# Performance work log

Hardware: AMD Instinct MI355X
Metric: run time of the kernel (lower is better)

## Reference

```python
import jax, jax.numpy as jnp
import numpy as np
from jax import lax

D_MODEL, D_STATE, D_CONV, EXPAND, HEADDIM = 1024, 128, 4, 2, 64
D_INNER = EXPAND * D_MODEL            # 2048
NHEADS = D_INNER // HEADDIM           # 32
CONV_DIM = D_INNER + 2 * D_STATE      # 2304 (ngroups=1)
D_IN_PROJ = 2 * D_INNER + 2 * D_STATE + NHEADS  # 4384


def setup_inputs() -> dict:
    key = jax.random.key(0)
    ks = jax.random.split(key, 9)
    b, l = 2, 2048
    x = jax.random.normal(ks[0], (b, l, D_MODEL), jnp.float32)
    in_proj_w = jax.random.normal(ks[1], (D_IN_PROJ, D_MODEL), jnp.float32) * 0.02
    conv_w = jax.random.normal(ks[2], (CONV_DIM, D_CONV), jnp.float32) * 0.2
    conv_b = jax.random.normal(ks[3], (CONV_DIM,), jnp.float32) * 0.02
    dt_bias = jnp.log(jnp.expm1(jax.random.uniform(ks[4], (NHEADS,), jnp.float32, 0.001, 0.1)))
    A_log = jnp.log(jax.random.uniform(ks[5], (NHEADS,), jnp.float32, 1.0, 16.0))
    D = jax.random.normal(ks[6], (NHEADS,), jnp.float32)
    norm_w = jnp.ones((D_INNER,), jnp.float32)
    out_proj_w = jax.random.normal(ks[7], (D_MODEL, D_INNER), jnp.float32) * 0.02
    return {"x": x, "in_proj_w": in_proj_w, "conv_w": conv_w, "conv_b": conv_b,
            "dt_bias": dt_bias, "A_log": A_log, "D": D, "norm_w": norm_w,
            "out_proj_w": out_proj_w}


def _mamba2(x, in_proj_w, conv_w, conv_b, dt_bias, A_log, D, norm_w, out_proj_w):
    b, l, _ = x.shape
    zxbcdt = x @ in_proj_w.T  # (b,l,D_IN_PROJ)
    z = zxbcdt[..., :D_INNER]
    xBC = zxbcdt[..., D_INNER:D_INNER + CONV_DIM]
    dt = zxbcdt[..., D_INNER + CONV_DIM:]  # (b,l,h)
    # causal depthwise conv1d + SiLU
    xBC_pad = jnp.pad(xBC, ((0, 0), (D_CONV - 1, 0), (0, 0)))
    windows = jnp.stack([xBC_pad[:, k:k + l, :] for k in range(D_CONV)], axis=-1)  # (b,l,c,K)
    xBC = jax.nn.silu(jnp.einsum('blck,ck->blc', windows, conv_w) + conv_b)
    xs = xBC[..., :D_INNER]
    B = xBC[..., D_INNER:D_INNER + D_STATE]   # (b,l,n)
    C = xBC[..., D_INNER + D_STATE:]          # (b,l,n)
    xh = xs.reshape(b, l, NHEADS, HEADDIM)
    dt = jax.nn.softplus(dt + dt_bias)        # (b,l,h)
    A = -jnp.exp(A_log)                       # (h,)
    dA = jnp.exp(dt * A)                      # (b,l,h)
    xdt = xh * dt[..., None]                  # (b,l,h,p)

    def step(S, inp):
        dA_t, xdt_t, B_t, C_t = inp  # (b,h),(b,h,p),(b,n),(b,n)
        S = dA_t[:, :, None, None] * S + xdt_t[..., None] * B_t[:, None, None, :]
        y_t = jnp.einsum('bhpn,bn->bhp', S, C_t)
        return S, y_t

    S0 = jnp.zeros((b, NHEADS, HEADDIM, D_STATE), x.dtype)
    _, y = lax.scan(step, S0,
                    (dA.transpose(1, 0, 2), xdt.transpose(1, 0, 2, 3),
                     B.transpose(1, 0, 2), C.transpose(1, 0, 2)))
    y = y.transpose(1, 0, 2, 3) + D[None, None, :, None] * xh  # (b,l,h,p)
    y = y.reshape(b, l, D_INNER)
    # gated RMSNorm: norm(y * silu(z)) * weight
    y = y * jax.nn.silu(z)
    y = y * lax.rsqrt(jnp.mean(y * y, axis=-1, keepdims=True) + 1e-5) * norm_w
    return y @ out_proj_w.T


def reference(x, in_proj_w, conv_w, conv_b, dt_bias, A_log, D, norm_w, out_proj_w):
    return x + _mamba2(x, in_proj_w, conv_w, conv_b, dt_bias, A_log, D, norm_w, out_proj_w)
```

## Files before the change

kernel.cpp:

```cpp
#include <hip/hip_runtime.h>
#include <hip/hip_bf16.h>
#include <cstdint>

typedef __hip_bfloat16 bf16;
typedef __attribute__((ext_vector_type(8))) short short8;
typedef __attribute__((ext_vector_type(4))) float f32x4;
typedef unsigned int u32;

#define BB 2
#define LL 2048
#define DM 1024
#define DI 2048
#define DS 128
#define NH 32
#define HD 64
#define CONVD 2304
#define DPROJ 4384
#define DPAD 4480
#define NBL (BB*LL)
#define NCHK 16
#define CLEN 128

__device__ __forceinline__ float bf2f(bf16 v) { return __bfloat162float(v); }
__device__ __forceinline__ bf16 f2bf(float f) { return __float2bfloat16(f); }
__device__ __forceinline__ unsigned short f2bfu(float f) {
  bf16 t = __float2bfloat16(f); return *(unsigned short*)&t;
}
__device__ __forceinline__ float bfu2f(unsigned short u) {
  u32 b = ((u32)u) << 16; return *(float*)&b;
}

__device__ __forceinline__ void gload16(const void* g, void* l) {
  __builtin_amdgcn_global_load_lds(
      (const __attribute__((address_space(1))) u32*)g,
      (__attribute__((address_space(3))) u32*)l, 16, 0, 0);
}

template<int N> __device__ __forceinline__ void waitvm() {
  __builtin_amdgcn_sched_barrier(0);
  if constexpr (N == 0) asm volatile("s_waitcnt vmcnt(0)" ::: "memory");
  else if constexpr (N == 3) asm volatile("s_waitcnt vmcnt(3)" ::: "memory");
  else if constexpr (N == 4) asm volatile("s_waitcnt vmcnt(4)" ::: "memory");
  __builtin_amdgcn_sched_barrier(0);
}
__device__ __forceinline__ void rawbar() {
  __builtin_amdgcn_sched_barrier(0);
  __builtin_amdgcn_s_barrier();
  __builtin_amdgcn_sched_barrier(0);
}

__global__ __launch_bounds__(256)
void k_cast3(const float* __restrict__ s0, bf16* __restrict__ d0, int n0,
             const float* __restrict__ s1, bf16* __restrict__ d1, int n1,
             const float* __restrict__ s2, bf16* __restrict__ d2, int n2)
{
  int i = blockIdx.x * blockDim.x + threadIdx.x;
  const int stride = gridDim.x * blockDim.x;
  const int total = n0 + n1 + n2;
  for (; i < total; i += stride) {
    const float* s; bf16* d; int j = i;
    if (j < n0)            { s = s0; d = d0; }
    else if (j < n0 + n1)  { s = s1; d = d1; j -= n0; }
    else                   { s = s2; d = d2; j -= n0 + n1; }
    const float4 v = ((const float4*)s)[j];
    u32 w0 = (u32)f2bfu(v.x) | ((u32)f2bfu(v.y) << 16);
    u32 w1 = (u32)f2bfu(v.z) | ((u32)f2bfu(v.w) << 16);
    *(uint2*)(d + (size_t)j*4) = make_uint2(w0, w1);
  }
}

template<int TM, int MODE>
__global__ __launch_bounds__(512)
void k_gemm_nt(const bf16* __restrict__ A, const bf16* __restrict__ W,
               int K, int Nw, int ldo,
               float* __restrict__ outf, const bf16* __restrict__ residb,
               bf16* __restrict__ outb, float* __restrict__ dtraw)
{
  constexpr int BUFE = (TM + 128) * 64;
  constexpr int LPT  = TM/64 + 2;
  __shared__ __align__(16) unsigned short S[3*BUFE];
  const int tid = threadIdx.x;
  const int w = tid >> 6, lane = tid & 63;
  const int m0 = blockIdx.x * TM, n0 = blockIdx.y * 128;
  const int wr = w >> 2, wc = w & 3;
  constexpr int MI = TM / 32;
  f32x4 acc[MI][2] = {};
  const int r0 = lane & 15;
  const int kq = (lane >> 4) * 8;
  const int srow = lane >> 3;
  const int scol = ((lane & 7) ^ (lane >> 3)) << 3;
  const int swz  = (r0 & 7) << 3;
  const int NT = K >> 6;

#define STAGE(T, BUF) {                                                          \
    const int k0s = (T) << 6;                                                    \
    unsigned short* dst = S + (BUF) * BUFE;                                      \
    _Pragma("unroll")                                                            \
    for (int it = 0; it < TM/64; ++it) {                                         \
      const int seg = it*8 + w;                                                  \
      const int row = seg*8 + srow;                                              \
      gload16(A + (size_t)(m0 + row)*K + (k0s + scol), (char*)dst + seg*1024);   \
    }                                                                            \
    unsigned short* dstW = dst + TM*64;                                          \
    _Pragma("unroll")                                                            \
    for (int it = 0; it < 2; ++it) {                                             \
      const int seg = it*8 + w;                                                  \
      const int row = seg*8 + srow;                                              \
      int rw = n0 + row; rw = (rw < Nw) ? rw : (Nw - 1);                         \
      gload16(W + (size_t)rw*K + (k0s + scol), (char*)dstW + seg*1024);          \
    }                                                                            \
  }

  STAGE(0, 0);
  STAGE(1, 1);
  waitvm<LPT>();
  rawbar();

  for (int t = 0; t < NT; ++t) {
    const int cur = t % 3;
    if (t + 2 < NT) STAGE(t + 2, (t + 2) % 3);
    const unsigned short* As = S + cur*BUFE;
    const unsigned short* Ws = As + TM*64;
    __builtin_amdgcn_s_setprio(1);
    #pragma unroll
    for (int kk = 0; kk < 64; kk += 32) {
      const int ce = (kk + kq) ^ swz;
      short8 af[MI], bw[2];
      #pragma unroll
      for (int mi = 0; mi < MI; ++mi)
        af[mi] = *(const short8*)(As + (wr*(TM/2) + mi*16 + r0)*64 + ce);
      #pragma unroll
      for (int ni = 0; ni < 2; ++ni)
        bw[ni] = *(const short8*)(Ws + (wc*32 + ni*16 + r0)*64 + ce);
      #pragma unroll
      for (int mi = 0; mi < MI; ++mi)
        #pragma unroll
        for (int ni = 0; ni < 2; ++ni)
          acc[mi][ni] = __builtin_amdgcn_mfma_f32_16x16x32_bf16(af[mi], bw[ni], acc[mi][ni], 0, 0, 0);
    }
    __builtin_amdgcn_s_setprio(0);
    if (t + 1 < NT) {
      if (t + 2 < NT) waitvm<LPT>();
      else            waitvm<0>();
      rawbar();
    }
  }
#undef STAGE

  const int rr = (lane >> 4) * 4;
  if (MODE == 0) {
    #pragma unroll
    for (int mi = 0; mi < MI; ++mi) {
      #pragma unroll
      for (int ni = 0; ni < 2; ++ni) {
        const int col = n0 + wc*32 + ni*16 + r0;
        #pragma unroll
        for (int r = 0; r < 4; ++r) {
          const int row = m0 + wr*(TM/2) + mi*16 + rr + r;
          outf[(size_t)row*ldo + col] =
              acc[mi][ni][r] + bf2f(residb[(size_t)row*ldo + col]);
        }
      }
    }
  } else {
    if (n0 == 4352 && wc == 0) {
      #pragma unroll
      for (int ni = 0; ni < 2; ++ni)
        #pragma unroll
        for (int mi = 0; mi < MI; ++mi)
          #pragma unroll
          for (int r = 0; r < 4; ++r) {
            const int row = m0 + wr*(TM/2) + mi*16 + rr + r;
            dtraw[(size_t)row*NH + ni*16 + r0] = acc[mi][ni][r];
          }
    }
    __syncthreads();
    #pragma unroll
    for (int mi = 0; mi < MI; ++mi) {
      #pragma unroll
      for (int ni = 0; ni < 2; ++ni) {
        const int colt = wc*32 + ni*16 + r0;
        #pragma unroll
        for (int r = 0; r < 4; ++r) {
          const int rowt = wr*(TM/2) + mi*16 + rr + r;
          const int g = (colt >> 3) ^ (rowt & 7);
          S[rowt*128 + g*8 + (colt & 7)] = f2bfu(acc[mi][ni][r]);
        }
      }
    }
    __syncthreads();
    const int row = tid >> 2, j4 = tid & 3;
    unsigned short* orow = (unsigned short*)outb + (size_t)(m0 + row)*ldo + n0 + j4*32;
    #pragma unroll
    for (int jj = 0; jj < 4; ++jj) {
      const int g = (j4*4 + jj) ^ (row & 7);
      *(short8*)(orow + jj*8) = *(const short8*)&S[row*128 + g*8];
    }
  }
}

__global__ __launch_bounds__(256)
void k_conv(const bf16* __restrict__ zxb, const float* __restrict__ dtraw,
            const float* __restrict__ convw, const float* __restrict__ convb,
            const float* __restrict__ dtb, const float* __restrict__ alog,
            bf16* __restrict__ xs, float* __restrict__ dt,
            float* __restrict__ ldA, bf16* __restrict__ Bc, bf16* __restrict__ Cc)
{
  const int bl = ((blockIdx.x & 7) << 9) | (blockIdx.x >> 3);
  const int l = bl & (LL - 1);
  const int tid = threadIdx.x;
  if (tid < NH) {
    float raw = dtraw[(size_t)bl*NH + tid] + dtb[tid];
    float sp = (raw > 20.f) ? raw : log1pf(__expf(raw));
    float Ah = -__expf(alog[tid]);
    dt[(size_t)bl*NH + tid] = sp;
    ldA[(size_t)bl*NH + tid] = sp * Ah;
  }
  for (int g = tid; g < CONVD/8; g += 256) {
    const int c0 = g*8;
    float acc[8];
    float4 wv[8];
    #pragma unroll
    for (int e = 0; e < 8; ++e) wv[e] = ((const float4*)convw)[c0 + e];
    {
      const float4 b0 = *(const float4*)(convb + c0);
      const float4 b1 = *(const float4*)(convb + c0 + 4);
      acc[0]=b0.x; acc[1]=b0.y; acc[2]=b0.z; acc[3]=b0.w;
      acc[4]=b1.x; acc[5]=b1.y; acc[6]=b1.z; acc[7]=b1.w;
    }
    #pragma unroll
    for (int k = 0; k < 4; ++k) {
      if (l - 3 + k >= 0) {
        short8 v = *(const short8*)((const unsigned short*)zxb + (size_t)(bl - 3 + k)*DPAD + DI + c0);
        #pragma unroll
        for (int e = 0; e < 8; ++e) {
          const float wk = (k == 0) ? wv[e].x : (k == 1) ? wv[e].y : (k == 2) ? wv[e].z : wv[e].w;
          acc[e] = fmaf(bfu2f((unsigned short)v[e]), wk, acc[e]);
        }
      }
    }
    short8 ov;
    #pragma unroll
    for (int e = 0; e < 8; ++e) {
      const float s = acc[e] / (1.f + __expf(-acc[e]));
      ov[e] = (short)f2bfu(s);
    }
    if (c0 < DI)            *(short8*)((unsigned short*)xs + (size_t)bl*DI + c0) = ov;
    else if (c0 < DI + DS)  *(short8*)((unsigned short*)Bc + (size_t)bl*DS + (c0 - DI)) = ov;
    else                    *(short8*)((unsigned short*)Cc + (size_t)bl*DS + (c0 - DI - DS)) = ov;
  }
}

__global__ __launch_bounds__(256)
void k_bt(const bf16* __restrict__ Bc, bf16* __restrict__ BT)
{
  const int bidx2 = blockIdx.x;
  const int b = bidx2 >> 4, c = bidx2 & 15;
  const int bl0 = b*LL + c*CLEN;
  __shared__ unsigned short LT[128*132];
  const int tid = threadIdx.x;
  {
    const int ts = tid >> 3, seg = tid & 7;
    #pragma unroll
    for (int r = 0; r < 4; ++r) {
      const int t = r*32 + ts;
      const unsigned short* src = (const unsigned short*)(Bc + (size_t)(bl0 + t)*DS);
      short8 v0 = *(const short8*)(src + seg*16);
      short8 v1 = *(const short8*)(src + seg*16 + 8);
      u32 w0 = (u32)(unsigned short)v0[0] | ((u32)(unsigned short)v0[1] << 16);
      u32 w1 = (u32)(unsigned short)v0[2] | ((u32)(unsigned short)v0[3] << 16);
      u32 w2 = (u32)(unsigned short)v0[4] | ((u32)(unsigned short)v0[5] << 16);
      u32 w3 = (u32)(unsigned short)v0[6] | ((u32)(unsigned short)v0[7] << 16);
      u32 w4 = (u32)(unsigned short)v1[0] | ((u32)(unsigned short)v1[1] << 16);
      u32 w5 = (u32)(unsigned short)v1[2] | ((u32)(unsigned short)v1[3] << 16);
      u32 w6 = (u32)(unsigned short)v1[4] | ((u32)(unsigned short)v1[5] << 16);
      u32 w7 = (u32)(unsigned short)v1[6] | ((u32)(unsigned short)v1[7] << 16);
      uint2* d = (uint2*)&LT[t*132 + seg*16];
      d[0] = make_uint2(w0, w1); d[1] = make_uint2(w2, w3);
      d[2] = make_uint2(w4, w5); d[3] = make_uint2(w6, w7);
    }
  }
  __syncthreads();
  {
    const int n = tid >> 1, th = tid & 1;
    unsigned short* dst = (unsigned short*)(BT + (size_t)bidx2*16384 + n*128 + th*64);
    #pragma unroll
    for (int j = 0; j < 8; ++j) {
      short8 o;
      #pragma unroll
      for (int e = 0; e < 8; ++e)
        o[e] = (short)LT[(th*64 + j*8 + e)*132 + n];
      *(short8*)(dst + j*8) = o;
    }
  }
}

__global__ __launch_bounds__(512)
void k_xt_state(const bf16* __restrict__ xs, const float* __restrict__ dt,
                const bf16* __restrict__ BT, const float* __restrict__ ldA,
                bf16* __restrict__ xT, unsigned short* __restrict__ Sloc,
                float* __restrict__ clog)
{
  const int bidx = blockIdx.x;
  const int c = bidx & 15, h = (bidx >> 4) & 31, b = bidx >> 9;
  const int bl0 = b*LL + c*CLEN;
  const int bidx2 = b*NCHK + c;
  __shared__ unsigned short LT[128*68];
  __shared__ __align__(16) unsigned short XWs[64*136];
  __shared__ float w1[128];
  const int tid = threadIdx.x;
  const int w = tid >> 6, lane = tid & 63;
  const int r0 = lane & 15, kq = (lane >> 4) * 8;
  short8 bfr[4];
  #pragma unroll
  for (int kk = 0; kk < 4; ++kk)
    bfr[kk] = *(const short8*)((const unsigned short*)BT + (size_t)bidx2*16384
                               + (size_t)(w*16 + r0)*128 + kk*32 + kq);
  {
    const int ts = tid >> 3, seg = tid & 7;
    #pragma unroll
    for (int r = 0; r < 2; ++r) {
      const int t = r*64 + ts;
      const float dtv = dt[(size_t)(bl0 + t)*NH + h];
      short8 v = *(const short8*)((const unsigned short*)(xs + (size_t)(bl0 + t)*DI + h*HD) + seg*8);
      unsigned short o[8];
      #pragma unroll
      for (int e = 0; e < 8; ++e)
        o[e] = f2bfu(bfu2f((unsigned short)v[e]) * dtv);
      uint2* d = (uint2*)&LT[t*68 + seg*8];
      d[0] = make_uint2((u32)o[0] | ((u32)o[1] << 16), (u32)o[2] | ((u32)o[3] << 16));
      d[1] = make_uint2((u32)o[4] | ((u32)o[5] << 16), (u32)o[6] | ((u32)o[7] << 16));
    }
  }
  if (tid < 64) {
    const int ln = tid;
    const float a0 = ldA[(size_t)(bl0 + 2*ln)*NH + h];
    const float a1 = ldA[(size_t)(bl0 + 2*ln + 1)*NH + h];
    float s = a0 + a1;
    #pragma unroll
    for (int off = 1; off < 64; off <<= 1) {
      const float v = __shfl_up(s, off);
      if (ln >= off) s += v;
    }
    const float Ltot = __shfl(s, 63);
    w1[2*ln + 1] = __expf(Ltot - s);
    w1[2*ln]     = __expf(Ltot - (s - a1));
    if (ln == 63) clog[bidx] = Ltot;
  }
  __syncthreads();
  {
    const int p = tid >> 3, tg = tid & 7;
    unsigned short* xdst = (unsigned short*)xT + (size_t)bidx*8192 + p*128 + tg*16;
    #pragma unroll
    for (int half = 0; half < 2; ++half) {
      short8 oXT, oXW;
      #pragma unroll
      for (int e = 0; e < 8; ++e) {
        const int t = tg*16 + half*8 + e;
        const unsigned short u = LT[t*68 + p];
        oXT[e] = (short)u;
        oXW[e] = (short)f2bfu(bfu2f(u) * w1[t]);
      }
      *(short8*)(xdst + half*8) = oXT;
      *(short8*)&XWs[p*136 + tg*16 + half*8] = oXW;
    }
  }
  __syncthreads();
  f32x4 acc[4] = {};
  #pragma unroll
  for (int kk = 0; kk < 4; ++kk) {
    #pragma unroll
    for (int mi = 0; mi < 4; ++mi) {
      short8 a = *(const short8*)&XWs[(mi*16 + r0)*136 + kk*32 + kq];
      acc[mi] = __builtin_amdgcn_mfma_f32_16x16x32_bf16(a, bfr[kk], acc[mi], 0, 0, 0);
    }
  }
  const int rr = (lane >> 4) * 4;
  unsigned short* So = Sloc + (size_t)bidx*8192;
  #pragma unroll
  for (int mi = 0; mi < 4; ++mi)
    #pragma unroll
    for (int r = 0; r < 4; ++r)
      So[(mi*16 + rr + r)*128 + w*16 + r0] = f2bfu(acc[mi][r]);
}

__global__ __launch_bounds__(256)
void k_chunk_combine(unsigned short* __restrict__ Sloc, const float* __restrict__ clog)
{
  const int bh = blockIdx.x >> 3;
  const int e0 = ((blockIdx.x & 7) * 256 + threadIdx.x) * 4;
  float t0 = 0.f, t1 = 0.f, t2 = 0.f, t3 = 0.f;
  for (int c = 0; c < NCHK; ++c) {
    unsigned short* Sp = Sloc + ((size_t)(bh*NCHK + c))*8192 + e0;
    const uint2 raw = *(const uint2*)Sp;
    const float l0 = bfu2f((unsigned short)(raw.x & 0xffff));
    const float l1 = bfu2f((unsigned short)(raw.x >> 16));
    const float l2 = bfu2f((unsigned short)(raw.y & 0xffff));
    const float l3 = bfu2f((unsigned short)(raw.y >> 16));
    uint2 o;
    o.x = (u32)f2bfu(t0) | ((u32)f2bfu(t1) << 16);
    o.y = (u32)f2bfu(t2) | ((u32)f2bfu(t3) << 16);
    *(uint2*)Sp = o;
    const float P = __expf(clog[bh*NCHK + c]);
    t0 = P*t0 + l0; t1 = P*t1 + l1; t2 = P*t2 + l2; t3 = P*t3 + l3;
  }
}

__global__ __launch_bounds__(512)
void k_scan(const bf16* __restrict__ xT, const bf16* __restrict__ Bc,
            const bf16* __restrict__ Cc, const unsigned short* __restrict__ Sinit,
            const float* __restrict__ ldA, const bf16* __restrict__ xs,
            const float* __restrict__ Dv, unsigned short* __restrict__ y)
{
  const int bidx = blockIdx.x;
  const int c = bidx & 15, h = (bidx >> 4) & 31, b = bidx >> 9;
  const int bl0 = b*LL + c*CLEN;
  __shared__ __align__(16) unsigned short Bs[128*136];
  __shared__ __align__(16) unsigned short XDs[64*136];
  __shared__ __align__(16) unsigned short SIs[64*136];
  __shared__ float la[128];
  const int tid = threadIdx.x;
  const int w = tid >> 6, lane = tid & 63;
  const int r0 = lane & 15, kq = (lane >> 4) * 8;
  short8 cfr[4];
  #pragma unroll
  for (int kk = 0; kk < 4; ++kk)
    cfr[kk] = *(const short8*)((const unsigned short*)Cc
                               + (size_t)(bl0 + w*16 + r0)*DS + kk*32 + kq);
  {
    const int t = tid >> 2, sg = tid & 3;
    const unsigned short* sb = (const unsigned short*)(Bc + (size_t)(bl0 + t)*DS) + sg*32;
    #pragma unroll
    for (int j = 0; j < 4; ++j)
      *(short8*)&Bs[t*136 + sg*32 + j*8] = *(const short8*)(sb + j*8);
  }
  {
    const int p = tid >> 3, seg = tid & 7;
    const unsigned short* sx = (const unsigned short*)(xT + (size_t)bidx*8192 + p*128) + seg*16;
    *(short8*)&XDs[p*136 + seg*16]     = *(const short8*)sx;
    *(short8*)&XDs[p*136 + seg*16 + 8] = *(const short8*)(sx + 8);
    const unsigned short* sp = Sinit + (size_t)bidx*8192 + p*128 + seg*16;
    *(short8*)&SIs[p*136 + seg*16]     = *(const short8*)sp;
    *(short8*)&SIs[p*136 + seg*16 + 8] = *(const short8*)(sp + 8);
  }
  if (tid < 64) {
    const int ln = tid;
    const float a0 = ldA[(size_t)(bl0 + 2*ln)*NH + h];
    const float a1 = ldA[(size_t)(bl0 + 2*ln + 1)*NH + h];
    float s = a0 + a1;
    #pragma unroll
    for (int off = 1; off < 64; off <<= 1) {
      const float v = __shfl_up(s, off);
      if (ln >= off) s += v;
    }
    la[2*ln + 1] = s;
    la[2*ln]     = s - a1;
  }
  __syncthreads();

  const int trow = w*16 + (lane >> 4) * 4;

  f32x4 aG[8] = {};
  f32x4 aU[4] = {};
  #pragma unroll
  for (int kk = 0; kk < 4; ++kk) {
    #pragma unroll
    for (int sf = 0; sf < 8; ++sf) {
      short8 bb = *(const short8*)&Bs[(sf*16 + r0)*136 + kk*32 + kq];
      aG[sf] = __builtin_amdgcn_mfma_f32_16x16x32_bf16(cfr[kk], bb, aG[sf], 0, 0, 0);
    }
    #pragma unroll
    for (int pf = 0; pf < 4; ++pf) {
      short8 bs = *(const short8*)&SIs[(pf*16 + r0)*136 + kk*32 + kq];
      aU[pf] = __builtin_amdgcn_mfma_f32_16x16x32_bf16(cfr[kk], bs, aU[pf], 0, 0, 0);
    }
  }
  __syncthreads();
  float lat[4];
  #pragma unroll
  for (int r = 0; r < 4; ++r) lat[r] = la[trow + r];
  #pragma unroll
  for (int sf = 0; sf < 8; ++sf) {
    const int s = sf*16 + r0;
    const float las = la[s];
    #pragma unroll
    for (int r = 0; r < 4; ++r) {
      const int t = trow + r;
      const float m = (s <= t) ? aG[sf][r] * __expf(lat[r] - las) : 0.f;
      Bs[t*136 + s] = f2bfu(m);
    }
  }
  __syncthreads();
  f32x4 aY[4] = {};
  #pragma unroll
  for (int kk = 0; kk < 4; ++kk) {
    short8 a = *(const short8*)&Bs[(w*16 + r0)*136 + kk*32 + kq];
    #pragma unroll
    for (int pf = 0; pf < 4; ++pf) {
      short8 bx = *(const short8*)&XDs[(pf*16 + r0)*136 + kk*32 + kq];
      aY[pf] = __builtin_amdgcn_mfma_f32_16x16x32_bf16(a, bx, aY[pf], 0, 0, 0);
    }
  }
  const float Dh = Dv[h];
  float el[4];
  #pragma unroll
  for (int r = 0; r < 4; ++r) el[r] = __expf(lat[r]);
  #pragma unroll
  for (int pf = 0; pf < 4; ++pf) {
    #pragma unroll
    for (int r = 0; r < 4; ++r) {
      const int t = trow + r, p = pf*16 + r0;
      const size_t gi = (size_t)(bl0 + t)*DI + h*HD + p;
      const float yv = aY[pf][r] + el[r]*aU[pf][r] + Dh*bfu2f(((const unsigned short*)xs)[gi]);
      y[gi] = f2bfu(yv);
    }
  }
}

__global__ __launch_bounds__(256)
void k_gate_norm(const unsigned short* __restrict__ y, const bf16* __restrict__ zxb,
                 const float* __restrict__ nw, bf16* __restrict__ yn)
{
  const size_t bl = blockIdx.x;
  const int tid = threadIdx.x;
  const int c0 = tid * 8;
  short8 yv8 = *(const short8*)(y + bl*DI + c0);
  short8 zv = *(const short8*)((const unsigned short*)zxb + bl*DPAD + c0);
  float v[8];
  float acc = 0.f;
  #pragma unroll
  for (int e = 0; e < 8; ++e) {
    const float zf = bfu2f((unsigned short)zv[e]);
    v[e] = bfu2f((unsigned short)yv8[e]) * (zf / (1.f + __expf(-zf)));
    acc += v[e]*v[e];
  }
  #pragma unroll
  for (int off = 32; off > 0; off >>= 1) acc += __shfl_down(acc, off);
  __shared__ float red[4];
  if ((tid & 63) == 0) red[tid >> 6] = acc;
  __syncthreads();
  const float total = red[0] + red[1] + red[2] + red[3];
  const float r = rsqrtf(total * (1.f/DI) + 1e-5f);
  const float4 w0 = *(const float4*)(nw + c0);
  const float4 w1 = *(const float4*)(nw + c0 + 4);
  const float wv[8] = {w0.x, w0.y, w0.z, w0.w, w1.x, w1.y, w1.z, w1.w};
  short8 ov;
  #pragma unroll
  for (int e = 0; e < 8; ++e) ov[e] = (short)f2bfu(v[e] * r * wv[e]);
  *(short8*)((unsigned short*)yn + bl*DI + c0) = ov;
}

extern "C" void kernel_launch(void* const* d_in, const int* in_sizes, int n_in,
                              void* d_out, int out_size, void* d_ws, size_t ws_size,
                              hipStream_t stream)
{
  const float* x     = (const float*)d_in[0];
  const float* inw   = (const float*)d_in[1];
  const float* convw = (const float*)d_in[2];
  const float* convb = (const float*)d_in[3];
  const float* dtb   = (const float*)d_in[4];
  const float* alog  = (const float*)d_in[5];
  const float* Dv    = (const float*)d_in[6];
  const float* nw    = (const float*)d_in[7];
  const float* outw  = (const float*)d_in[8];
  float* out = (float*)d_out;
  char* ws = (char*)d_ws;

  constexpr size_t OFF_ZX   = 0;
  constexpr size_t OFF_DTRAW= OFF_ZX   + (size_t)NBL*DPAD*2;
  constexpr size_t OFF_XS   = OFF_DTRAW+ (size_t)NBL*NH*4;
  constexpr size_t OFF_DT   = OFF_XS   + (size_t)NBL*DI*2;
  constexpr size_t OFF_LDA  = OFF_DT   + (size_t)NBL*NH*4;
  constexpr size_t OFF_B    = OFF_LDA  + (size_t)NBL*NH*4;
  constexpr size_t OFF_C    = OFF_B    + (size_t)NBL*DS*2;
  constexpr size_t OFF_XT   = OFF_C    + (size_t)NBL*DS*2;
  constexpr size_t OFF_BT   = OFF_XT   + (size_t)1024*8192*2;
  constexpr size_t OFF_SLOC = OFF_BT   + (size_t)32*16384*2;
  constexpr size_t OFF_CLOG = OFF_SLOC + (size_t)1024*8192*2;
  constexpr size_t OFF_Y    = OFF_CLOG + 4096;
  constexpr size_t OFF_YN   = OFF_Y    + (size_t)NBL*DI*2;
  constexpr size_t OFF_XB   = OFF_YN   + (size_t)NBL*DI*2;
  constexpr size_t OFF_INWB = OFF_XB   + (size_t)NBL*DM*2;
  constexpr size_t OFF_OUTWB= OFF_INWB + (size_t)DPROJ*DM*2;

  bf16*  zxb  = (bf16*) (ws + OFF_ZX);
  float* dtraw= (float*)(ws + OFF_DTRAW);
  bf16*  xs   = (bf16*) (ws + OFF_XS);
  float* dt   = (float*)(ws + OFF_DT);
  float* ldA  = (float*)(ws + OFF_LDA);
  bf16*  Bcp  = (bf16*) (ws + OFF_B);
  bf16*  Ccp  = (bf16*) (ws + OFF_C);
  bf16*  xT   = (bf16*) (ws + OFF_XT);
  bf16*  BT   = (bf16*) (ws + OFF_BT);
  unsigned short* Sloc = (unsigned short*)(ws + OFF_SLOC);
  float* clog = (float*)(ws + OFF_CLOG);
  unsigned short* yb = (unsigned short*)(ws + OFF_Y);
  bf16*  yn   = (bf16*) (ws + OFF_YN);
  bf16*  xb   = (bf16*) (ws + OFF_XB);
  bf16*  inwb = (bf16*) (ws + OFF_INWB);
  bf16*  outwb= (bf16*) (ws + OFF_OUTWB);

  k_cast3<<<2048, 256, 0, stream>>>(x, xb, NBL*DM/4,
                                    inw, inwb, DPROJ*DM/4,
                                    outw, outwb, DM*DI/4);
  k_gemm_nt<128,1><<<dim3(32, 35), 512, 0, stream>>>(xb, inwb, DM, DPROJ, DPAD, nullptr, nullptr, zxb, dtraw);
  k_conv<<<NBL, 256, 0, stream>>>(zxb, dtraw, convw, convb, dtb, alog, xs, dt, ldA, Bcp, Ccp);
  k_bt<<<BB*NCHK, 256, 0, stream>>>(Bcp, BT);
  k_xt_state<<<BB*NH*NCHK, 512, 0, stream>>>(xs, dt, BT, ldA, xT, Sloc, clog);
  k_chunk_combine<<<64*8, 256, 0, stream>>>(Sloc, clog);
  k_scan<<<BB*NH*NCHK, 512, 0, stream>>>(xT, Bcp, Ccp, Sloc, ldA, xs, Dv, yb);
  k_gate_norm<<<NBL, 256, 0, stream>>>(yb, zxb, nw, yn);
  k_gemm_nt<64,0><<<dim3(64, 8), 512, 0, stream>>>(yn, outwb, DI, DM, DM, out, xb, nullptr, nullptr);
}
```

Measured before the change: 203.9 us.

## Load in-projection A operand directly to registers and raise MFMA priority in scan kernels

Adds a dedicated in-projection GEMM kernel that loads the activation tile straight from global memory into registers, double-buffered across even and odd K steps. Only the weight tile is staged through LDS, which shrinks LDS use and may allow more resident blocks (launch bounds now request 4). The scan and state kernels also wrap their MFMA loops in s_setprio to favour matrix issue. The cost is higher register pressure from direct global loads, which are not coalesced the way the LDS staging was.

```diff
diff --git a/kernel.cpp b/kernel.cpp
--- a/kernel.cpp
+++ b/kernel.cpp
@@ -39,6 +39,7 @@
 template<int N> __device__ __forceinline__ void waitvm() {
   __builtin_amdgcn_sched_barrier(0);
   if constexpr (N == 0) asm volatile("s_waitcnt vmcnt(0)" ::: "memory");
+  else if constexpr (N == 2) asm volatile("s_waitcnt vmcnt(2)" ::: "memory");
   else if constexpr (N == 3) asm volatile("s_waitcnt vmcnt(3)" ::: "memory");
   else if constexpr (N == 4) asm volatile("s_waitcnt vmcnt(4)" ::: "memory");
   __builtin_amdgcn_sched_barrier(0);
@@ -69,12 +70,138 @@
   }
 }
 
-template<int TM, int MODE>
+__global__ __launch_bounds__(512, 4)
+void k_gemm_in(const bf16* __restrict__ A, const bf16* __restrict__ W,
+               bf16* __restrict__ outb, float* __restrict__ dtraw)
+{
+  constexpr int K  = DM;
+  constexpr int NT = K >> 6;
+  constexpr int WB = 128*64;
+  __shared__ __align__(16) unsigned short Sw[3*WB];
+  const int tid = threadIdx.x;
+  const int w = tid >> 6, lane = tid & 63;
+  const int m0 = blockIdx.x * 128, n0 = blockIdx.y * 128;
+  const int wr = w >> 2, wc = w & 3;
+  f32x4 acc[4][2] = {};
+  const int r0 = lane & 15;
+  const int kq = (lane >> 4) * 8;
+  const int srow = lane >> 3;
+  const int scol = ((lane & 7) ^ (lane >> 3)) << 3;
+  const int swz  = (r0 & 7) << 3;
+
+  const unsigned short* Arow[4];
+  #pragma unroll
+  for (int mi = 0; mi < 4; ++mi)
+    Arow[mi] = (const unsigned short*)A + (size_t)(m0 + wr*64 + mi*16 + r0)*K + kq;
+
+#define LOADA(T, DST) {                                                \
+    const int k0a = (T) << 6;                                          \
+    _Pragma("unroll")                                                  \
+    for (int mi = 0; mi < 4; ++mi) {                                   \
+      DST[mi][0] = *(const short8*)(Arow[mi] + k0a);                   \
+      DST[mi][1] = *(const short8*)(Arow[mi] + k0a + 32);              \
+    }                                                                  \
+  }
+#define STAGEW(T, BUF) {                                               \
+    const int k0s = (T) << 6;                                          \
+    unsigned short* dst = Sw + (BUF)*WB;                               \
+    _Pragma("unroll")                                                  \
+    for (int it = 0; it < 2; ++it) {                                   \
+      const int seg = it*8 + w;                                        \
+      const int row = seg*8 + srow;                                    \
+      int rw = n0 + row; rw = (rw < DPROJ) ? rw : (DPROJ - 1);         \
+      gload16(W + (size_t)rw*K + (k0s + scol), (char*)dst + seg*1024); \
+    }                                                                  \
+  }
+#define COMPUTE(AR, BUF) {                                             \
+    const unsigned short* Ws_ = Sw + (BUF)*WB;                         \
+    _Pragma("unroll")                                                  \
+    for (int kk2 = 0; kk2 < 2; ++kk2) {                                \
+      const int ce = (kk2*32 + kq) ^ swz;                              \
+      short8 bw[2];                                                    \
+      _Pragma("unroll")                                                \
+      for (int ni = 0; ni < 2; ++ni)                                   \
+        bw[ni] = *(const short8*)(Ws_ + (wc*32 + ni*16 + r0)*64 + ce); \
+      _Pragma("unroll")                                                \
+      for (int mi = 0; mi < 4; ++mi)                                   \
+        _Pragma("unroll")                                              \
+        for (int ni = 0; ni < 2; ++ni)                                 \
+          acc[mi][ni] = __builtin_amdgcn_mfma_f32_16x16x32_bf16(AR[mi][kk2], bw[ni], acc[mi][ni], 0, 0, 0); \
+    }                                                                  \
+  }
+
+  short8 aEv[4][2], aOd[4][2];
+  LOADA(0, aEv);
+  STAGEW(0, 0);
+  STAGEW(1, 1);
+  waitvm<2>();
+  rawbar();
+
+  for (int t = 0; t < NT; t += 2) {
+    if (t + 1 < NT) LOADA(t + 1, aOd);
+    if (t + 2 < NT) STAGEW(t + 2, (t + 2) % 3);
+    COMPUTE(aEv, t % 3);
+    if (t + 1 < NT) {
+      if (t + 2 < NT) waitvm<2>();
+      else            waitvm<0>();
+      rawbar();
+    }
+    if (t + 1 < NT) {
+      if (t + 2 < NT) LOADA(t + 2, aEv);
+      if (t + 3 < NT) STAGEW(t + 3, (t + 3) % 3);
+      COMPUTE(aOd, (t + 1) % 3);
+      if (t + 2 < NT) {
+        if (t + 3 < NT) waitvm<2>();
+        else            waitvm<0>();
+        rawbar();
+      }
+    }
+  }
+#undef LOADA
+#undef STAGEW
+#undef COMPUTE
+
+  const int rr = (lane >> 4) * 4;
+  if (n0 == 4352 && wc == 0) {
+    #pragma unroll
+    for (int ni = 0; ni < 2; ++ni)
+      #pragma unroll
+      for (int mi = 0; mi < 4; ++mi)
+        #pragma unroll
+        for (int r = 0; r < 4; ++r) {
+          const int row = m0 + wr*64 + mi*16 + rr + r;
+          dtraw[(size_t)row*NH + ni*16 + r0] = acc[mi][ni][r];
+        }
+  }
+  __syncthreads();
+  #pragma unroll
+  for (int mi = 0; mi < 4; ++mi) {
+    #pragma unroll
+    for (int ni = 0; ni < 2; ++ni) {
+      const int colt = wc*32 + ni*16 + r0;
+      #pragma unroll
+      for (int r = 0; r < 4; ++r) {
+        const int rowt = wr*64 + mi*16 + rr + r;
+        const int g = (colt >> 3) ^ (rowt & 7);
+        Sw[rowt*128 + g*8 + (colt & 7)] = f2bfu(acc[mi][ni][r]);
+      }
+    }
+  }
+  __syncthreads();
+  const int row = tid >> 2, j4 = tid & 3;
+  unsigned short* orow = (unsigned short*)outb + (size_t)(m0 + row)*DPAD + n0 + j4*32;
+  #pragma unroll
+  for (int jj = 0; jj < 4; ++jj) {
+    const int g = (j4*4 + jj) ^ (row & 7);
+    *(short8*)(orow + jj*8) = *(const short8*)&Sw[row*128 + g*8];
+  }
+}
+
+template<int TM>
 __global__ __launch_bounds__(512)
-void k_gemm_nt(const bf16* __restrict__ A, const bf16* __restrict__ W,
-               int K, int Nw, int ldo,
-               float* __restrict__ outf, const bf16* __restrict__ residb,
-               bf16* __restrict__ outb, float* __restrict__ dtraw)
+void k_gemm_out(const bf16* __restrict__ A, const bf16* __restrict__ W,
+                int K, int Nw, int ldo,
+                float* __restrict__ outf, const bf16* __restrict__ residb)
 {
   constexpr int BUFE = (TM + 128) * 64;
   constexpr int LPT  = TM/64 + 2;
@@ -148,53 +275,17 @@
 #undef STAGE
 
   const int rr = (lane >> 4) * 4;
-  if (MODE == 0) {
-    #pragma unroll
-    for (int mi = 0; mi < MI; ++mi) {
-      #pragma unroll
-      for (int ni = 0; ni < 2; ++ni) {
-        const int col = n0 + wc*32 + ni*16 + r0;
-        #pragma unroll
-        for (int r = 0; r < 4; ++r) {
-          const int row = m0 + wr*(TM/2) + mi*16 + rr + r;
-          outf[(size_t)row*ldo + col] =
-              acc[mi][ni][r] + bf2f(residb[(size_t)row*ldo + col]);
-        }
+  #pragma unroll
+  for (int mi = 0; mi < MI; ++mi) {
+    #pragma unroll
+    for (int ni = 0; ni < 2; ++ni) {
+      const int col = n0 + wc*32 + ni*16 + r0;
+      #pragma unroll
+      for (int r = 0; r < 4; ++r) {
+        const int row = m0 + wr*(TM/2) + mi*16 + rr + r;
+        outf[(size_t)row*ldo + col] =
+            acc[mi][ni][r] + bf2f(residb[(size_t)row*ldo + col]);
       }
-    }
-  } else {
-    if (n0 == 4352 && wc == 0) {
-      #pragma unroll
-      for (int ni = 0; ni < 2; ++ni)
-        #pragma unroll
-        for (int mi = 0; mi < MI; ++mi)
-          #pragma unroll
-          for (int r = 0; r < 4; ++r) {
-            const int row = m0 + wr*(TM/2) + mi*16 + rr + r;
-            dtraw[(size_t)row*NH + ni*16 + r0] = acc[mi][ni][r];
-          }
-    }
-    __syncthreads();
-    #pragma unroll
-    for (int mi = 0; mi < MI; ++mi) {
-      #pragma unroll
-      for (int ni = 0; ni < 2; ++ni) {
-        const int colt = wc*32 + ni*16 + r0;
-        #pragma unroll
-        for (int r = 0; r < 4; ++r) {
-          const int rowt = wr*(TM/2) + mi*16 + rr + r;
-          const int g = (colt >> 3) ^ (rowt & 7);
-          S[rowt*128 + g*8 + (colt & 7)] = f2bfu(acc[mi][ni][r]);
-        }
-      }
-    }
-    __syncthreads();
-    const int row = tid >> 2, j4 = tid & 3;
-    unsigned short* orow = (unsigned short*)outb + (size_t)(m0 + row)*ldo + n0 + j4*32;
-    #pragma unroll
-    for (int jj = 0; jj < 4; ++jj) {
-      const int g = (j4*4 + jj) ^ (row & 7);
-      *(short8*)(orow + jj*8) = *(const short8*)&S[row*128 + g*8];
     }
   }
 }
@@ -367,6 +458,7 @@
   }
   __syncthreads();
   f32x4 acc[4] = {};
+  __builtin_amdgcn_s_setprio(1);
   #pragma unroll
   for (int kk = 0; kk < 4; ++kk) {
     #pragma unroll
@@ -375,6 +467,7 @@
       acc[mi] = __builtin_amdgcn_mfma_f32_16x16x32_bf16(a, bfr[kk], acc[mi], 0, 0, 0);
     }
   }
+  __builtin_amdgcn_s_setprio(0);
   const int rr = (lane >> 4) * 4;
   unsigned short* So = Sloc + (size_t)bidx*8192;
   #pragma unroll
@@ -462,6 +555,7 @@
 
   f32x4 aG[8] = {};
   f32x4 aU[4] = {};
+  __builtin_amdgcn_s_setprio(1);
   #pragma unroll
   for (int kk = 0; kk < 4; ++kk) {
     #pragma unroll
@@ -475,6 +569,7 @@
       aU[pf] = __builtin_amdgcn_mfma_f32_16x16x32_bf16(cfr[kk], bs, aU[pf], 0, 0, 0);
     }
   }
+  __builtin_amdgcn_s_setprio(0);
   __syncthreads();
   float lat[4];
   #pragma unroll
@@ -492,6 +587,7 @@
   }
   __syncthreads();
   f32x4 aY[4] = {};
+  __builtin_amdgcn_s_setprio(1);
   #pragma unroll
   for (int kk = 0; kk < 4; ++kk) {
     short8 a = *(const short8*)&Bs[(w*16 + r0)*136 + kk*32 + kq];
@@ -501,6 +597,7 @@
       aY[pf] = __builtin_amdgcn_mfma_f32_16x16x32_bf16(a, bx, aY[pf], 0, 0, 0);
     }
   }
+  __builtin_amdgcn_s_setprio(0);
   const float Dh = Dv[h];
   float el[4];
   #pragma unroll
@@ -603,12 +700,12 @@
   k_cast3<<<2048, 256, 0, stream>>>(x, xb, NBL*DM/4,
                                     inw, inwb, DPROJ*DM/4,
                                     outw, outwb, DM*DI/4);
-  k_gemm_nt<128,1><<<dim3(32, 35), 512, 0, stream>>>(xb, inwb, DM, DPROJ, DPAD, nullptr, nullptr, zxb, dtraw);
+  k_gemm_in<<<dim3(32, 35), 512, 0, stream>>>(xb, inwb, zxb, dtraw);
   k_conv<<<NBL, 256, 0, stream>>>(zxb, dtraw, convw, convb, dtb, alog, xs, dt, ldA, Bcp, Ccp);
   k_bt<<<BB*NCHK, 256, 0, stream>>>(Bcp, BT);
   k_xt_state<<<BB*NH*NCHK, 512, 0, stream>>>(xs, dt, BT, ldA, xT, Sloc, clog);
   k_chunk_combine<<<64*8, 256, 0, stream>>>(Sloc, clog);
   k_scan<<<BB*NH*NCHK, 512, 0, stream>>>(xT, Bcp, Ccp, Sloc, ldA, xs, Dv, yb);
   k_gate_norm<<<NBL, 256, 0, stream>>>(yb, zxb, nw, yn);
-  k_gemm_nt<64,0><<<dim3(64, 8), 512, 0, stream>>>(yn, outwb, DI, DM, DM, out, xb, nullptr, nullptr);
-}
+  k_gemm_out<64><<<dim3(64, 8), 512, 0, stream>>>(yn, outwb, DI, DM, DM, out, xb);
+}
```

Measured after the change: 296.6 us. +45.5%, slower.
